# Kernel tuning notes

Measured on AMD Instinct MI355X. Metric: run time of the kernel, lower is better.

## Reference

```python
import jax, jax.numpy as jnp
import numpy as np

HIDDEN = 1024
HEADS = 16
HEAD_DIM = HIDDEN // HEADS
SEQ = 2048
BATCH = 2


def setup_inputs() -> dict:
    key = jax.random.key(0)
    ks = jax.random.split(key, 11)
    s = 1.0 / np.sqrt(HIDDEN)
    inp = {
        'query': jax.random.normal(ks[0], (SEQ, BATCH, HIDDEN), jnp.float32),
        'key': jax.random.normal(ks[1], (SEQ, BATCH, HIDDEN), jnp.float32),
        'value': jax.random.normal(ks[2], (SEQ, BATCH, HIDDEN), jnp.float32),
        'Wq': jax.random.normal(ks[3], (HIDDEN, HIDDEN), jnp.float32) * s,
        'bq': jnp.zeros((HIDDEN,), jnp.float32),
        'Wk': jax.random.normal(ks[4], (HIDDEN, HIDDEN), jnp.float32) * s,
        'bk': jnp.zeros((HIDDEN,), jnp.float32),
        'Wv': jax.random.normal(ks[5], (HIDDEN, HIDDEN), jnp.float32) * s,
        'bv': jnp.zeros((HIDDEN,), jnp.float32),
        'Wo': jax.random.normal(ks[6], (HIDDEN, HIDDEN), jnp.float32) * s,
        'bo': jnp.zeros((HIDDEN,), jnp.float32),
    }
    return inp


def reference(query, key, value, Wq, bq, Wk, bk, Wv, bv, Wo, bo):
    # Linear layers: torch Linear computes x @ W.T + b
    S, B, _ = query.shape
    q = (query @ Wq.T + bq).reshape(S, B, HEADS, HEAD_DIM)
    k = (key @ Wk.T + bk).reshape(S, B, HEADS, HEAD_DIM)
    v = (value @ Wv.T + bv).reshape(S, B, HEADS, HEAD_DIM)
    # -> [B, H, S, D]
    q = jnp.transpose(q, (1, 2, 0, 3))
    k = jnp.transpose(k, (1, 2, 0, 3))
    v = jnp.transpose(v, (1, 2, 0, 3))
    scores = jnp.einsum('bhqd,bhkd->bhqk', q, k) / np.sqrt(HEAD_DIM)
    attn = jax.nn.softmax(scores, axis=-1)  # dropout=0.0 -> identity
    out = jnp.einsum('bhqk,bhkd->bhqd', attn, v)
    out = jnp.transpose(out, (2, 0, 1, 3)).reshape(S, B, HIDDEN)
    out = out @ Wo.T + bo
    return out, attn
```

## Files before the change

kernel.cpp:

```cpp
#include <hip/hip_runtime.h>
#include <hip/hip_bf16.h>
#include <cstdint>
#include <cstddef>

#define SEQLEN 2048
#define NBATCH 2
#define NHEAD  16
#define HDIM   64
#define HID    1024
#define MROWS  4096

typedef __bf16 bf16x8 __attribute__((ext_vector_type(8)));
typedef float f32x4 __attribute__((ext_vector_type(4)));
typedef unsigned short ushort8 __attribute__((ext_vector_type(8)));

#define MFMA16(a, b, c) __builtin_amdgcn_mfma_f32_16x16x32_bf16((a), (b), (c), 0, 0, 0)

#define GLOAD_LDS16(g, l)                                                        \
    __builtin_amdgcn_global_load_lds(                                            \
        (const __attribute__((address_space(1))) void*)(g),                      \
        (__attribute__((address_space(3))) void*)(l), 16, 0, 0)

#define SBAR() __builtin_amdgcn_s_barrier()
#define SCHED_FENCE() __builtin_amdgcn_sched_barrier(0)
#define WAIT_VMCNT(n) asm volatile("s_waitcnt vmcnt(" #n ")" ::: "memory")

static __device__ __forceinline__ unsigned int pack_bf16_pair(float lo, float hi) {
    unsigned short a = __builtin_bit_cast(unsigned short, (__bf16)lo);
    unsigned short b = __builtin_bit_cast(unsigned short, (__bf16)hi);
    return ((unsigned int)b << 16) | a;
}

__global__ __launch_bounds__(256) void conv6(
    const float* __restrict__ s0, const float* __restrict__ s1, const float* __restrict__ s2,
    const float* __restrict__ s3, const float* __restrict__ s4, const float* __restrict__ s5,
    unsigned short* __restrict__ Sc)
{
    const int y = blockIdx.y;
    const float* src = (y == 0) ? s0 : (y == 1) ? s1 : (y == 2) ? s2
                     : (y == 3) ? s3 : (y == 4) ? s4 : s5;
    const size_t M1 = 1u << 20;
    unsigned short* dst = (y < 3) ? (Sc + (size_t)y * 4 * M1) : (Sc + 12 * M1 + (size_t)(y - 3) * M1);
    const size_t n = (y < 3) ? 4 * M1 : M1;

    const size_t i = ((size_t)blockIdx.x * 256 + threadIdx.x) * 8;
    if (i >= n) return;
    float4 f0 = *(const float4*)(src + i);
    float4 f1 = *(const float4*)(src + i + 4);
    ushort8 o;
    o[0] = __builtin_bit_cast(unsigned short, (__bf16)f0.x);
    o[1] = __builtin_bit_cast(unsigned short, (__bf16)f0.y);
    o[2] = __builtin_bit_cast(unsigned short, (__bf16)f0.z);
    o[3] = __builtin_bit_cast(unsigned short, (__bf16)f0.w);
    o[4] = __builtin_bit_cast(unsigned short, (__bf16)f1.x);
    o[5] = __builtin_bit_cast(unsigned short, (__bf16)f1.y);
    o[6] = __builtin_bit_cast(unsigned short, (__bf16)f1.z);
    o[7] = __builtin_bit_cast(unsigned short, (__bf16)f1.w);
    *(ushort8*)(dst + i) = o;
}

__global__ __launch_bounds__(256) void wconv(
    const float* __restrict__ Wo, unsigned short* __restrict__ Wob)
{
    const size_t i = ((size_t)blockIdx.x * 256 + threadIdx.x) * 8;
    float4 f0 = *(const float4*)(Wo + i);
    float4 f1 = *(const float4*)(Wo + i + 4);
    ushort8 o;
    o[0] = __builtin_bit_cast(unsigned short, (__bf16)f0.x);
    o[1] = __builtin_bit_cast(unsigned short, (__bf16)f0.y);
    o[2] = __builtin_bit_cast(unsigned short, (__bf16)f0.z);
    o[3] = __builtin_bit_cast(unsigned short, (__bf16)f0.w);
    o[4] = __builtin_bit_cast(unsigned short, (__bf16)f1.x);
    o[5] = __builtin_bit_cast(unsigned short, (__bf16)f1.y);
    o[6] = __builtin_bit_cast(unsigned short, (__bf16)f1.z);
    o[7] = __builtin_bit_cast(unsigned short, (__bf16)f1.w);
    *(ushort8*)(Wob + i) = o;
}

#define GSTAGE32(DSTARR, SRCP, k0v)                                              \
    _Pragma("unroll")                                                            \
    for (int c_ = 0; c_ < 2; ++c_) {                                             \
        const int row_ = (c_ << 6) + (threadIdx.x >> 2);                         \
        const unsigned short* gs_ = (SRCP) + (size_t)row_ * HID + (k0v)          \
            + ((((int)threadIdx.x & 3) ^ ((row_ >> 1) & 3)) << 3);               \
        GLOAD_LDS16(gs_, &(DSTARR)[((c_ << 6) + (((int)threadIdx.x >> 6) << 4)) * 32]); \
    }

#define GEMM_BODY(ApT, BpT)                                                      \
    GSTAGE32(As[0], ApT, 0);                                                     \
    GSTAGE32(Bs[0], BpT, 0);                                                     \
    for (int it = 0; it < 32; ++it) {                                            \
        SBAR();                                                                  \
        const int k1 = ((it + 1) & 31) << 5;                                     \
        GSTAGE32(As[(it + 1) & 1], ApT, k1);                                     \
        GSTAGE32(Bs[(it + 1) & 1], BpT, k1);                                     \
        WAIT_VMCNT(8);                                                           \
        SBAR();                                                                  \
        SCHED_FENCE();                                                           \
        const char* Ac = (const char*)As[it & 1];                                \
        const char* Bc = (const char*)Bs[it & 1];                                \
        bf16x8 a_h[4], b_h[4];                                                   \
        _Pragma("unroll")                                                        \
        for (int m = 0; m < 4; ++m) {                                            \
            const int row = wm * 64 + m * 16 + fr;                               \
            a_h[m] = *(const bf16x8*)(Ac + (row << 6) + ((fg ^ ((row >> 1) & 3)) << 4)); \
        }                                                                        \
        _Pragma("unroll")                                                        \
        for (int n = 0; n < 4; ++n) {                                            \
            const int row = wn * 64 + n * 16 + fr;                               \
            b_h[n] = *(const bf16x8*)(Bc + (row << 6) + ((fg ^ ((row >> 1) & 3)) << 4)); \
        }                                                                        \
        __builtin_amdgcn_s_setprio(1);                                           \
        _Pragma("unroll")                                                        \
        for (int m = 0; m < 4; ++m)                                              \
            _Pragma("unroll")                                                    \
            for (int n = 0; n < 4; ++n)                                          \
                acc[m][n] = MFMA16(a_h[m], b_h[n], acc[m][n]);                   \
        __builtin_amdgcn_s_setprio(0);                                           \
    }

__global__ __launch_bounds__(256) void qkv_gemm(
    const unsigned short* __restrict__ Sc,
    const float* __restrict__ bq, const float* __restrict__ bk, const float* __restrict__ bv,
    unsigned short* __restrict__ Qb, unsigned short* __restrict__ Kb, unsigned short* __restrict__ Vb)
{
    const int z = blockIdx.z;
    const size_t M1 = 1u << 20;
    const unsigned short* A = Sc + (size_t)z * 4 * M1;
    const unsigned short* B = Sc + 12 * M1 + (size_t)z * M1;
    const float* bias = (z == 0) ? bq : (z == 1) ? bk : bv;
    unsigned short* dst = (z == 0) ? Qb : (z == 1) ? Kb : Vb;

    __shared__ unsigned short As[2][128 * 32];
    __shared__ unsigned short Bs[2][128 * 32];

    const int t = threadIdx.x, lane = t & 63, w = t >> 6;
    const int wm = w >> 1, wn = w & 1;
    const int bm = blockIdx.x * 128, bn = blockIdx.y * 128;
    const int fr = lane & 15, fg = lane >> 4;

    const unsigned short* Ap = A + (size_t)bm * HID;
    const unsigned short* Bp = B + (size_t)bn * HID;

    f32x4 acc[4][4] = {};
    GEMM_BODY(Ap, Bp)

    #pragma unroll
    for (int n = 0; n < 4; ++n) {
        const int gc = bn + wn * 64 + n * 16 + fr;
        const float bb = bias[gc];
        #pragma unroll
        for (int m = 0; m < 4; ++m)
            #pragma unroll
            for (int r = 0; r < 4; ++r) {
                const int gr = bm + wm * 64 + m * 16 + fg * 4 + r;
                *(__bf16*)&dst[(size_t)gr * HID + gc] = (__bf16)(acc[m][n][r] + bb);
            }
    }
}

__global__ __launch_bounds__(256) void vtrans(
    const unsigned short* __restrict__ Vb, unsigned short* __restrict__ Vt)
{
    __shared__ unsigned short T[64][66];
    const int t = threadIdx.x;
    const int s0 = blockIdx.x * 64, h = blockIdx.y, b = blockIdx.z;

    {
        const int s_l = t >> 2, d0 = (t & 3) * 16;
        const unsigned short* src = Vb + (((size_t)(s0 + s_l) * 2 + b) << 10) + (h << 6) + d0;
        *(ushort8*)&T[s_l][d0]     = *(const ushort8*)src;
        *(ushort8*)&T[s_l][d0 + 8] = *(const ushort8*)(src + 8);
    }
    __syncthreads();
    {
        const int d_l = t >> 2, sc = (t & 3) * 16;
        ushort8 o0, o1;
        #pragma unroll
        for (int j = 0; j < 8; ++j) { o0[j] = T[sc + j][d_l]; o1[j] = T[sc + 8 + j][d_l]; }
        unsigned short* dst = Vt + (((size_t)((b << 4) + h) * 64 + d_l) << 11) + s0 + sc;
        *(ushort8*)dst       = o0;
        *(ushort8*)(dst + 8) = o1;
    }
}

#define STAGE_K(ktv, bufsel)                                                     \
    {                                                                            \
        const int kti_ = (ktv) & 15;                                             \
        _Pragma("unroll")                                                        \
        for (int c_ = 0; c_ < 4; ++c_) {                                         \
            const int rb_ = (w << 5) + (c_ << 3);                                \
            const int rl_ = rb_ + (lane >> 3);                                   \
            const unsigned short* ks_ = Kb + (((size_t)((kti_ << 7) + rl_) * 2 + b) << 10) \
                + (h << 6) + (((lane & 7) ^ (rl_ & 7)) << 3);                    \
            GLOAD_LDS16(ks_, &Ks[bufsel][rb_ * 64]);                             \
        }                                                                        \
    }

__global__ __launch_bounds__(256) void attn2(
    const unsigned short* __restrict__ Qb, const unsigned short* __restrict__ Kb,
    const unsigned short* __restrict__ Vt, float* __restrict__ attn_out,
    unsigned short* __restrict__ Hb)
{
    __shared__ unsigned short Ks[2][128 * 64];
    __shared__ unsigned short Pl[4][16 * 128];

    const int flat = blockIdx.x + (blockIdx.y << 4) + (blockIdx.z << 8);
    const int nf = (flat & 7) * 64 + (flat >> 3);
    const int qblk = nf & 15, h = (nf >> 4) & 15, b = nf >> 8;

    const int t = threadIdx.x, lane = t & 63, w = t >> 6;
    const int fr = lane & 15, fg = lane >> 4;
    const int fg4 = fg << 2, fg16 = fg << 4;
    const int qbase = qblk * 128 + w * 32;
    const float c_exp = 0.18033688011112042f;

    bf16x8 qf[2][2];
    #pragma unroll
    for (int mi = 0; mi < 2; ++mi) {
        const int q = qbase + mi * 16 + fr;
        const unsigned short* qp = Qb + (((size_t)q * 2 + b) << 10) + (h << 6);
        qf[mi][0] = *(const bf16x8*)(qp + (fg << 3));
        qf[mi][1] = *(const bf16x8*)(qp + 32 + (fg << 3));
    }

    char* Plc = (char*)&Pl[w][0];
    float lsum[2] = {0.f, 0.f};

    STAGE_K(0, 0);
    for (int kt = 0; kt < 16; ++kt) {
        SBAR();
        STAGE_K(kt + 1, (kt + 1) & 1);
        WAIT_VMCNT(4);
        SBAR();
        SCHED_FENCE();

        const char* Kc = (const char*)Ks[kt & 1];
        f32x4 s_[2][8] = {};
        __builtin_amdgcn_s_setprio(1);
        #pragma unroll
        for (int n = 0; n < 8; ++n) {
            const int row = (n << 4) + fr;
            const int rx = (row & 7) << 4;
            #pragma unroll
            for (int kk = 0; kk < 2; ++kk) {
                bf16x8 kf = *(const bf16x8*)(Kc + (row << 7) + (((kk << 6) | fg16) ^ rx));
                s_[0][n] = MFMA16(kf, qf[0][kk], s_[0][n]);
                s_[1][n] = MFMA16(kf, qf[1][kk], s_[1][n]);
            }
        }
        __builtin_amdgcn_s_setprio(0);

        #pragma unroll
        for (int mi = 0; mi < 2; ++mi) {
            float a = 0.f;
            #pragma unroll
            for (int n = 0; n < 8; ++n)
                #pragma unroll
                for (int r = 0; r < 4; ++r)
                    a += exp2f(s_[mi][n][r] * c_exp);
            lsum[mi] += a;
        }
    }

    float li[2];
    #pragma unroll
    for (int mi = 0; mi < 2; ++mi) {
        float v = lsum[mi];
        v += __shfl_xor(v, 16);
        v += __shfl_xor(v, 32);
        li[mi] = -__log2f(v);
    }

    f32x4 oacc[2][4] = {};
    float* attnB = attn_out + ((size_t)((b << 4) + h) << 22);
    const size_t vhead = (size_t)((b << 4) + h) << 6;

    for (int kt = 0; kt < 16; ++kt) {
        SBAR();
        STAGE_K(kt + 1, (kt + 1) & 1);
        WAIT_VMCNT(4);
        SBAR();
        SCHED_FENCE();

        const char* Kc = (const char*)Ks[kt & 1];
        f32x4 s_[2][8] = {};
        __builtin_amdgcn_s_setprio(1);
        #pragma unroll
        for (int n = 0; n < 8; ++n) {
            const int row = (n << 4) + fr;
            const int rx = (row & 7) << 4;
            #pragma unroll
            for (int kk = 0; kk < 2; ++kk) {
                bf16x8 kf = *(const bf16x8*)(Kc + (row << 7) + (((kk << 6) | fg16) ^ rx));
                s_[0][n] = MFMA16(kf, qf[0][kk], s_[0][n]);
                s_[1][n] = MFMA16(kf, qf[1][kk], s_[1][n]);
            }
        }
        __builtin_amdgcn_s_setprio(0);

        const int rxl = (fr & 7) << 4;
        #pragma unroll
        for (int mi = 0; mi < 2; ++mi) {
            float* ab = attnB + ((size_t)(qbase + (mi << 4) + fr) << 11) + (kt << 7) + fg4;
            #pragma unroll
            for (int n = 0; n < 8; ++n) {
                f32x4 p;
                #pragma unroll
                for (int r = 0; r < 4; ++r)
                    p[r] = exp2f(__builtin_fmaf(s_[mi][n][r], c_exp, li[mi]));
                __builtin_nontemporal_store(p, (f32x4*)(ab + (n << 4)));
                uint2 pk;
                pk.x = pack_bf16_pair(p[0], p[1]);
                pk.y = pack_bf16_pair(p[2], p[3]);
                *(uint2*)(Plc + (fr << 8) + (((n << 5) | (fg << 3)) ^ rxl)) = pk;
            }
            asm volatile("s_waitcnt lgkmcnt(0)" ::: "memory");
            SCHED_FENCE();

            __builtin_amdgcn_s_setprio(1);
            #pragma unroll
            for (int kk2 = 0; kk2 < 4; ++kk2) {
                bf16x8 pa = *(const bf16x8*)(Plc + (fr << 8) + (((kk2 << 6) | fg16) ^ rxl));
                #pragma unroll
                for (int n2 = 0; n2 < 4; ++n2) {
                    bf16x8 vf = *(const bf16x8*)(Vt + ((vhead + (n2 << 4) + fr) << 11)
                                                 + (kt << 7) + (kk2 << 5) + (fg << 3));
                    oacc[mi][n2] = MFMA16(pa, vf, oacc[mi][n2]);
                }
            }
            __builtin_amdgcn_s_setprio(0);
        }
    }

    #pragma unroll
    for (int mi = 0; mi < 2; ++mi)
        #pragma unroll
        for (int n2 = 0; n2 < 4; ++n2)
            #pragma unroll
            for (int r = 0; r < 4; ++r) {
                const int q = qbase + (mi << 4) + fg4 + r;
                *(__bf16*)&Hb[(((size_t)q * 2 + b) << 10) + (h << 6) + (n2 << 4) + fr] =
                    (__bf16)oacc[mi][n2][r];
            }
}

__global__ __launch_bounds__(256) void out_proj(
    const unsigned short* __restrict__ Hb, const unsigned short* __restrict__ Wob,
    const float* __restrict__ bo, float* __restrict__ out)
{
    __shared__ unsigned short As[2][128 * 32];
    __shared__ unsigned short Bs[2][128 * 32];

    const int t = threadIdx.x, lane = t & 63, w = t >> 6;
    const int wm = w >> 1, wn = w & 1;
    const int bm = blockIdx.x * 128, bn = blockIdx.y * 128;
    const int fr = lane & 15, fg = lane >> 4;

    const unsigned short* Ap = Hb + (size_t)bm * HID;
    const unsigned short* Bp = Wob + (size_t)bn * HID;

    f32x4 acc[4][4] = {};
    GEMM_BODY(Ap, Bp)

    #pragma unroll
    for (int n = 0; n < 4; ++n) {
        const int gc = bn + wn * 64 + n * 16 + fr;
        const float bb = bo[gc];
        #pragma unroll
        for (int m = 0; m < 4; ++m)
            #pragma unroll
            for (int r = 0; r < 4; ++r) {
                const int gr = bm + wm * 64 + m * 16 + fg * 4 + r;
                out[(size_t)gr * HID + gc] = acc[m][n][r] + bb;
            }
    }
}

extern "C" void kernel_launch(void* const* d_in, const int* in_sizes, int n_in,
                              void* d_out, int out_size, void* d_ws, size_t ws_size,
                              hipStream_t stream)
{
    (void)in_sizes; (void)n_in; (void)out_size;

    const float* query = (const float*)d_in[0];
    const float* key   = (const float*)d_in[1];
    const float* value = (const float*)d_in[2];
    const float* bq    = (const float*)d_in[4];
    const float* bk    = (const float*)d_in[6];
    const float* bv    = (const float*)d_in[8];
    const float* Wo    = (const float*)d_in[9];
    const float* bo    = (const float*)d_in[10];

    float* out0 = (float*)d_out;
    float* attn = out0 + (size_t)MROWS * HID;

    if (ws_size < (size_t)32 * 1024 * 1024) return;
    const size_t nbuf = (size_t)MROWS * HID;
    unsigned short* Qb = (unsigned short*)d_ws;
    unsigned short* Kb = Qb + nbuf;
    unsigned short* Vb = Kb + nbuf;
    unsigned short* Vt = Vb + nbuf;
    unsigned short* Hb = Vb;
    unsigned short* Wob = Qb;

    unsigned short* Sc = (unsigned short*)attn;

    conv6<<<dim3(2048, 6), 256, 0, stream>>>(query, key, value,
                                             (const float*)d_in[3], (const float*)d_in[5],
                                             (const float*)d_in[7], Sc);
    qkv_gemm<<<dim3(32, 8, 3), 256, 0, stream>>>(Sc, bq, bk, bv, Qb, Kb, Vb);
    vtrans<<<dim3(32, NHEAD, NBATCH), 256, 0, stream>>>(Vb, Vt);
    attn2<<<dim3(16, NHEAD, NBATCH), 256, 0, stream>>>(Qb, Kb, Vt, attn, Hb);
    wconv<<<dim3(512), 256, 0, stream>>>(Wo, Wob);
    out_proj<<<dim3(32, 8), 256, 0, stream>>>(Hb, Wob, bo, out0);
}
```

Measured before the change: 319.0 us.

## Halve attention query tile, single-buffer K, and use regular attn stores

The attention kernel now processes 64 query rows per block (16 per wave) instead of 128, doubling the grid to 1024 blocks. K staging drops from double buffering with async prefetch to a single LDS buffer loaded synchronously between two __syncthreads. The attention-probability stores switch from nontemporal to ordinary stores, and the explicit lgkmcnt wait before reading P back is removed. The aim is more parallelism and lower register and LDS use per block, at the cost of reloading K twice as often and losing the overlap of K loads with compute.

```diff
diff --git a/kernel.cpp b/kernel.cpp
--- a/kernel.cpp
+++ b/kernel.cpp
@@ -184,16 +184,16 @@
     }
 }
 
-#define STAGE_K(ktv, bufsel)                                                     \
+#define STAGE_K1(ktv)                                                            \
     {                                                                            \
-        const int kti_ = (ktv) & 15;                                             \
+        const int kti_ = (ktv);                                                  \
         _Pragma("unroll")                                                        \
         for (int c_ = 0; c_ < 4; ++c_) {                                         \
             const int rb_ = (w << 5) + (c_ << 3);                                \
             const int rl_ = rb_ + (lane >> 3);                                   \
             const unsigned short* ks_ = Kb + (((size_t)((kti_ << 7) + rl_) * 2 + b) << 10) \
                 + (h << 6) + (((lane & 7) ^ (rl_ & 7)) << 3);                    \
-            GLOAD_LDS16(ks_, &Ks[bufsel][rb_ * 64]);                             \
+            GLOAD_LDS16(ks_, &Ks[rb_ * 64]);                                     \
         }                                                                        \
     }
 
@@ -202,41 +202,37 @@
     const unsigned short* __restrict__ Vt, float* __restrict__ attn_out,
     unsigned short* __restrict__ Hb)
 {
-    __shared__ unsigned short Ks[2][128 * 64];
+    __shared__ unsigned short Ks[128 * 64];
     __shared__ unsigned short Pl[4][16 * 128];
 
-    const int flat = blockIdx.x + (blockIdx.y << 4) + (blockIdx.z << 8);
-    const int nf = (flat & 7) * 64 + (flat >> 3);
-    const int qblk = nf & 15, h = (nf >> 4) & 15, b = nf >> 8;
+    const int flat = blockIdx.x + (blockIdx.y << 5) + (blockIdx.z << 9);
+    const int nf = (flat & 7) * 128 + (flat >> 3);
+    const int qblk = nf & 31, h = (nf >> 5) & 15, b = nf >> 9;
 
     const int t = threadIdx.x, lane = t & 63, w = t >> 6;
     const int fr = lane & 15, fg = lane >> 4;
     const int fg4 = fg << 2, fg16 = fg << 4;
-    const int qbase = qblk * 128 + w * 32;
+    const int qbase = qblk * 64 + w * 16;
     const float c_exp = 0.18033688011112042f;
 
-    bf16x8 qf[2][2];
-    #pragma unroll
-    for (int mi = 0; mi < 2; ++mi) {
-        const int q = qbase + mi * 16 + fr;
+    bf16x8 qf[2];
+    {
+        const int q = qbase + fr;
         const unsigned short* qp = Qb + (((size_t)q * 2 + b) << 10) + (h << 6);
-        qf[mi][0] = *(const bf16x8*)(qp + (fg << 3));
-        qf[mi][1] = *(const bf16x8*)(qp + 32 + (fg << 3));
+        qf[0] = *(const bf16x8*)(qp + (fg << 3));
+        qf[1] = *(const bf16x8*)(qp + 32 + (fg << 3));
     }
 
     char* Plc = (char*)&Pl[w][0];
-    float lsum[2] = {0.f, 0.f};
-
-    STAGE_K(0, 0);
+    float lsum = 0.f;
+
     for (int kt = 0; kt < 16; ++kt) {
-        SBAR();
-        STAGE_K(kt + 1, (kt + 1) & 1);
-        WAIT_VMCNT(4);
-        SBAR();
-        SCHED_FENCE();
-
-        const char* Kc = (const char*)Ks[kt & 1];
-        f32x4 s_[2][8] = {};
+        __syncthreads();
+        STAGE_K1(kt);
+        __syncthreads();
+
+        const char* Kc = (const char*)Ks;
+        f32x4 s_[8] = {};
         __builtin_amdgcn_s_setprio(1);
         #pragma unroll
         for (int n = 0; n < 8; ++n) {
@@ -245,46 +241,40 @@
             #pragma unroll
             for (int kk = 0; kk < 2; ++kk) {
                 bf16x8 kf = *(const bf16x8*)(Kc + (row << 7) + (((kk << 6) | fg16) ^ rx));
-                s_[0][n] = MFMA16(kf, qf[0][kk], s_[0][n]);
-                s_[1][n] = MFMA16(kf, qf[1][kk], s_[1][n]);
+                s_[n] = MFMA16(kf, qf[kk], s_[n]);
             }
         }
         __builtin_amdgcn_s_setprio(0);
 
-        #pragma unroll
-        for (int mi = 0; mi < 2; ++mi) {
-            float a = 0.f;
-            #pragma unroll
-            for (int n = 0; n < 8; ++n)
-                #pragma unroll
-                for (int r = 0; r < 4; ++r)
-                    a += exp2f(s_[mi][n][r] * c_exp);
-            lsum[mi] += a;
-        }
-    }
-
-    float li[2];
-    #pragma unroll
-    for (int mi = 0; mi < 2; ++mi) {
-        float v = lsum[mi];
+        float a = 0.f;
+        #pragma unroll
+        for (int n = 0; n < 8; ++n)
+            #pragma unroll
+            for (int r = 0; r < 4; ++r)
+                a += exp2f(s_[n][r] * c_exp);
+        lsum += a;
+    }
+
+    float li;
+    {
+        float v = lsum;
         v += __shfl_xor(v, 16);
         v += __shfl_xor(v, 32);
-        li[mi] = -__log2f(v);
-    }
-
-    f32x4 oacc[2][4] = {};
+        li = -__log2f(v);
+    }
+
+    f32x4 oacc[4] = {};
     float* attnB = attn_out + ((size_t)((b << 4) + h) << 22);
     const size_t vhead = (size_t)((b << 4) + h) << 6;
+    const int rxl = (fr & 7) << 4;
 
     for (int kt = 0; kt < 16; ++kt) {
-        SBAR();
-        STAGE_K(kt + 1, (kt + 1) & 1);
-        WAIT_VMCNT(4);
-        SBAR();
-        SCHED_FENCE();
-
-        const char* Kc = (const char*)Ks[kt & 1];
-        f32x4 s_[2][8] = {};
+        __syncthreads();
+        STAGE_K1(kt);
+        __syncthreads();
+
+        const char* Kc = (const char*)Ks;
+        f32x4 s_[8] = {};
         __builtin_amdgcn_s_setprio(1);
         #pragma unroll
         for (int n = 0; n < 8; ++n) {
@@ -293,56 +283,47 @@
             #pragma unroll
             for (int kk = 0; kk < 2; ++kk) {
                 bf16x8 kf = *(const bf16x8*)(Kc + (row << 7) + (((kk << 6) | fg16) ^ rx));
-                s_[0][n] = MFMA16(kf, qf[0][kk], s_[0][n]);
-                s_[1][n] = MFMA16(kf, qf[1][kk], s_[1][n]);
+                s_[n] = MFMA16(kf, qf[kk], s_[n]);
             }
         }
         __builtin_amdgcn_s_setprio(0);
 
-        const int rxl = (fr & 7) << 4;
-        #pragma unroll
-        for (int mi = 0; mi < 2; ++mi) {
-            float* ab = attnB + ((size_t)(qbase + (mi << 4) + fr) << 11) + (kt << 7) + fg4;
-            #pragma unroll
-            for (int n = 0; n < 8; ++n) {
-                f32x4 p;
-                #pragma unroll
-                for (int r = 0; r < 4; ++r)
-                    p[r] = exp2f(__builtin_fmaf(s_[mi][n][r], c_exp, li[mi]));
-                __builtin_nontemporal_store(p, (f32x4*)(ab + (n << 4)));
-                uint2 pk;
-                pk.x = pack_bf16_pair(p[0], p[1]);
-                pk.y = pack_bf16_pair(p[2], p[3]);
-                *(uint2*)(Plc + (fr << 8) + (((n << 5) | (fg << 3)) ^ rxl)) = pk;
-            }
-            asm volatile("s_waitcnt lgkmcnt(0)" ::: "memory");
-            SCHED_FENCE();
-
-            __builtin_amdgcn_s_setprio(1);
-            #pragma unroll
-            for (int kk2 = 0; kk2 < 4; ++kk2) {
-                bf16x8 pa = *(const bf16x8*)(Plc + (fr << 8) + (((kk2 << 6) | fg16) ^ rxl));
-                #pragma unroll
-                for (int n2 = 0; n2 < 4; ++n2) {
-                    bf16x8 vf = *(const bf16x8*)(Vt + ((vhead + (n2 << 4) + fr) << 11)
-                                                 + (kt << 7) + (kk2 << 5) + (fg << 3));
-                    oacc[mi][n2] = MFMA16(pa, vf, oacc[mi][n2]);
-                }
-            }
-            __builtin_amdgcn_s_setprio(0);
-        }
+        float* ab = attnB + ((size_t)(qbase + fr) << 11) + (kt << 7) + fg4;
+        #pragma unroll
+        for (int n = 0; n < 8; ++n) {
+            f32x4 p;
+            #pragma unroll
+            for (int r = 0; r < 4; ++r)
+                p[r] = exp2f(__builtin_fmaf(s_[n][r], c_exp, li));
+            *(f32x4*)(ab + (n << 4)) = p;
+            uint2 pk;
+            pk.x = pack_bf16_pair(p[0], p[1]);
+            pk.y = pack_bf16_pair(p[2], p[3]);
+            *(uint2*)(Plc + (fr << 8) + (((n << 5) | (fg << 3)) ^ rxl)) = pk;
+        }
+
+        __builtin_amdgcn_s_setprio(1);
+        #pragma unroll
+        for (int kk2 = 0; kk2 < 4; ++kk2) {
+            bf16x8 pa = *(const bf16x8*)(Plc + (fr << 8) + (((kk2 << 6) | fg16) ^ rxl));
+            #pragma unroll
+            for (int n2 = 0; n2 < 4; ++n2) {
+                bf16x8 vf = *(const bf16x8*)(Vt + ((vhead + (n2 << 4) + fr) << 11)
+                                             + (kt << 7) + (kk2 << 5) + (fg << 3));
+                oacc[n2] = MFMA16(pa, vf, oacc[n2]);
+            }
+        }
+        __builtin_amdgcn_s_setprio(0);
     }
 
     #pragma unroll
-    for (int mi = 0; mi < 2; ++mi)
-        #pragma unroll
-        for (int n2 = 0; n2 < 4; ++n2)
-            #pragma unroll
-            for (int r = 0; r < 4; ++r) {
-                const int q = qbase + (mi << 4) + fg4 + r;
-                *(__bf16*)&Hb[(((size_t)q * 2 + b) << 10) + (h << 6) + (n2 << 4) + fr] =
-                    (__bf16)oacc[mi][n2][r];
-            }
+    for (int n2 = 0; n2 < 4; ++n2)
+        #pragma unroll
+        for (int r = 0; r < 4; ++r) {
+            const int q = qbase + fg4 + r;
+            *(__bf16*)&Hb[(((size_t)q * 2 + b) << 10) + (h << 6) + (n2 << 4) + fr] =
+                (__bf16)oacc[n2][r];
+        }
 }
 
 __global__ __launch_bounds__(256) void out_proj(
@@ -411,7 +392,7 @@
                                              (const float*)d_in[7], Sc);
     qkv_gemm<<<dim3(32, 8, 3), 256, 0, stream>>>(Sc, bq, bk, bv, Qb, Kb, Vb);
     vtrans<<<dim3(32, NHEAD, NBATCH), 256, 0, stream>>>(Vb, Vt);
-    attn2<<<dim3(16, NHEAD, NBATCH), 256, 0, stream>>>(Qb, Kb, Vt, attn, Hb);
+    attn2<<<dim3(32, NHEAD, NBATCH), 256, 0, stream>>>(Qb, Kb, Vt, attn, Hb);
     wconv<<<dim3(512), 256, 0, stream>>>(Wo, Wob);
     out_proj<<<dim3(32, 8), 256, 0, stream>>>(Hb, Wob, bo, out0);
 }
```

Result: slower. 338.8 us (+6.2%).
